# Kernel tuning notes

Measured on AMD Instinct MI355X. Metric: run time of the kernel, lower is better.

The kernel has to match this reference:

```python
import jax, jax.numpy as jnp
import numpy as np

N = 200_000        # atoms
E = 800_000        # directed edges (pairs e, e^1 are mutual reverses)
H = 512            # hidden_size
AF = 133           # atom_feat_size
BF = 14            # bond_feat_size
B = 4096           # num graphs


def setup_inputs() -> dict:
    key = jax.random.key(0)
    ks = jax.random.split(key, 8)
    atom_hiddens = jax.random.normal(ks[0], (N, H), dtype=jnp.float32)
    # undirected bonds, then interleave as (src,dst),(dst,src) so rev[e] = e ^ 1
    src = jax.random.randint(ks[1], (E // 2,), 0, N, dtype=jnp.int32)
    dst = jax.random.randint(ks[2], (E // 2,), 0, N, dtype=jnp.int32)
    heads = jnp.stack([src, dst], axis=1).reshape(-1)   # [E]
    tails = jnp.stack([dst, src], axis=1).reshape(-1)   # [E]
    edge_index = jnp.stack([heads, tails], axis=0)      # [2, E]
    rev_edge_index = jnp.arange(E, dtype=jnp.int32) ^ 1
    batch = jnp.sort(jax.random.randint(ks[3], (N,), 0, B, dtype=jnp.int32))
    batch = batch.at[-1].set(B - 1)  # batch[-1]+1 == B, matching the torch code
    s = 1.0 / np.sqrt(H)
    return {
        "atom_hiddens": atom_hiddens,
        "W_node": jax.random.normal(ks[4], (H, AF), dtype=jnp.float32) * s,
        "b_node": jnp.zeros((AF,), dtype=jnp.float32),
        "W_edge": jax.random.normal(ks[5], (H, BF), dtype=jnp.float32) * s,
        "b_edge": jnp.zeros((BF,), dtype=jnp.float32),
        "W_g1": jax.random.normal(ks[6], (H, H), dtype=jnp.float32) * s,
        "b_g1": jnp.zeros((H,), dtype=jnp.float32),
        "W_g2": jax.random.normal(ks[7], (H, 1), dtype=jnp.float32) * s,
        "b_g2": jnp.zeros((1,), dtype=jnp.float32),
        "edge_index": edge_index,
        "rev_edge_index": rev_edge_index,
        "batch": batch,
        "num_graphs": B,
    }


def reference(atom_hiddens, W_node, b_node, W_edge, b_edge, W_g1, b_g1,
              W_g2, b_g2, edge_index, rev_edge_index, batch, num_graphs):
    # graph pooling: index_add_ over the sorted batch vector
    graph_emb = jax.ops.segment_sum(atom_hiddens, batch, num_segments=num_graphs)
    # node head
    node_pred = atom_hiddens @ W_node + b_node
    # edge dedup: the torch loop keeps edge e iff its reverse was not yet
    # visited, i.e. iff e < rev_edge_index[e] (rev is an involution), giving
    # exactly E//2 kept edges.
    e_ids = jnp.arange(edge_index.shape[1])
    keep = jnp.nonzero(e_ids < rev_edge_index, size=edge_index.shape[1] // 2,
                       fill_value=0)[0]
    a1 = edge_index[0, keep]
    a2 = edge_index[1, keep]
    bond_emb = 0.5 * (atom_hiddens[a1] + atom_hiddens[a2])  # [E//2, H]
    edge_pred = bond_emb @ W_edge + b_edge
    # graph head: Linear -> ReLU -> Linear
    graph_pred = jax.nn.relu(graph_emb @ W_g1 + b_g1) @ W_g2 + b_g2
    return node_pred, edge_pred, graph_pred
```

## Files before the change

kernel.cpp:

```cpp
#include <hip/hip_runtime.h>

#define NATOMS 200000
#define NEDGE  800000
#define NBOND  400000
#define HDIM   512
#define AF     133
#define BFEAT  14
#define NGRAPH 4096

#define NODE_OUT_SZ (NATOMS * AF)
#define EDGE_OUT_SZ (NBOND * BFEAT)

#define WS_P     0
#define WS_BMAT  12800000
#define WS_BIAS  12963840
#define WS_GE    12964480
#define WS_WG1T  17158784

typedef _Float16 half8 __attribute__((ext_vector_type(8)));
typedef float floatx4 __attribute__((ext_vector_type(4)));

__global__ void pack_kernel(const float* __restrict__ Wn, const float* __restrict__ bn,
                            const float* __restrict__ We, const float* __restrict__ be,
                            const float* __restrict__ Wg1, const float* __restrict__ bg2,
                            _Float16* __restrict__ Bmat, float* __restrict__ bias,
                            _Float16* __restrict__ Wg1t, float* __restrict__ gpred) {
    int idx = blockIdx.x * 256 + threadIdx.x;
    if (idx < 160 * 512) {
        int n = idx >> 9, k = idx & 511;
        float v = 0.f;
        if (n < AF)              v = Wn[k * AF + n];
        else if (n < AF + BFEAT) v = We[k * BFEAT + (n - AF)];
        Bmat[idx] = (_Float16)v;
    } else if (idx < 160 * 512 + 512 * 512) {
        int i = idx - 160 * 512;
        int n = i >> 9, k = i & 511;
        Wg1t[i] = (_Float16)Wg1[k * HDIM + n];
    } else if (idx < 160 * 512 + 512 * 512 + 160) {
        int n = idx - (160 * 512 + 512 * 512);
        float v = 0.f;
        if (n < AF)              v = bn[n];
        else if (n < AF + BFEAT) v = be[n - AF];
        bias[n] = v;
    } else if (idx < 160 * 512 + 512 * 512 + 160 + NGRAPH) {
        gpred[idx - (160 * 512 + 512 * 512 + 160)] = bg2[0];
    }
}

__global__ __launch_bounds__(256) void pool_kernel(const float* __restrict__ A,
                                                   const int* __restrict__ batch,
                                                   _Float16* __restrict__ GE) {
    int g = blockIdx.x;
    int t = threadIdx.x;
    int lo = 0, hi = NATOMS;
    while (lo < hi) { int mid = (lo + hi) >> 1; if (batch[mid] < g) lo = mid + 1; else hi = mid; }
    int start = lo;
    hi = NATOMS;
    while (lo < hi) { int mid = (lo + hi) >> 1; if (batch[mid] < g + 1) lo = mid + 1; else hi = mid; }
    int end = lo;
    float s0 = 0.f, s1 = 0.f;
    for (int i = start; i < end; ++i) {
        s0 += A[(size_t)i * HDIM + t];
        s1 += A[(size_t)i * HDIM + t + 256];
    }
    GE[(size_t)g * HDIM + t]       = (_Float16)s0;
    GE[(size_t)g * HDIM + t + 256] = (_Float16)s1;
}

__global__ __launch_bounds__(256) void gemm_node(const float* __restrict__ A,
                                                 const _Float16* __restrict__ Bm,
                                                 const float* __restrict__ bias,
                                                 float* __restrict__ node_out,
                                                 float* __restrict__ P) {
    __shared__ _Float16 As[128][72];
    __shared__ _Float16 Bs[160][72];

    const int t    = threadIdx.x;
    const int bm   = blockIdx.x;
    const int w    = t >> 6, l = t & 63, quad = l >> 4, lr = l & 15;
    const int wm   = w & 1, wn = w >> 1;

    floatx4 acc[4][5];
    for (int mt = 0; mt < 4; ++mt)
        for (int nt = 0; nt < 5; ++nt)
            acc[mt][nt] = (floatx4){0.f, 0.f, 0.f, 0.f};

    const int arow0 = t >> 2;
    const int aseg  = (t & 3) * 16;

    for (int ko = 0; ko < 8; ++ko) {
        const int k0 = ko * 64;
        float4 av[2][4];
        for (int p = 0; p < 2; ++p) {
            int row = arow0 + p * 64;
            long grow = (long)bm * 128 + row;
            if (grow < NATOMS) {
                const float4* src = (const float4*)(A + grow * HDIM + k0 + aseg);
                av[p][0] = src[0]; av[p][1] = src[1]; av[p][2] = src[2]; av[p][3] = src[3];
            } else {
                av[p][0] = av[p][1] = av[p][2] = av[p][3] = make_float4(0.f, 0.f, 0.f, 0.f);
            }
        }
        uint4 bv[5];
        for (int it = 0; it < 5; ++it) {
            int idx = t + it * 256;
            int row = idx >> 3, c = (idx & 7) * 8;
            bv[it] = *(const uint4*)(Bm + row * HDIM + k0 + c);
        }
        __syncthreads();
        for (int p = 0; p < 2; ++p) {
            int row = arow0 + p * 64;
            half8 h0 = {(_Float16)av[p][0].x, (_Float16)av[p][0].y, (_Float16)av[p][0].z, (_Float16)av[p][0].w,
                        (_Float16)av[p][1].x, (_Float16)av[p][1].y, (_Float16)av[p][1].z, (_Float16)av[p][1].w};
            half8 h1 = {(_Float16)av[p][2].x, (_Float16)av[p][2].y, (_Float16)av[p][2].z, (_Float16)av[p][2].w,
                        (_Float16)av[p][3].x, (_Float16)av[p][3].y, (_Float16)av[p][3].z, (_Float16)av[p][3].w};
            *(half8*)&As[row][aseg]     = h0;
            *(half8*)&As[row][aseg + 8] = h1;
        }
        for (int it = 0; it < 5; ++it) {
            int idx = t + it * 256;
            int row = idx >> 3, c = (idx & 7) * 8;
            *(uint4*)&Bs[row][c] = bv[it];
        }
        __syncthreads();
        for (int kk = 0; kk < 64; kk += 32) {
            half8 af[4], bf[5];
            for (int mt = 0; mt < 4; ++mt)
                af[mt] = *(const half8*)&As[wm * 64 + mt * 16 + lr][kk + quad * 8];
            for (int nt = 0; nt < 5; ++nt)
                bf[nt] = *(const half8*)&Bs[wn * 80 + nt * 16 + lr][kk + quad * 8];
            for (int mt = 0; mt < 4; ++mt)
                for (int nt = 0; nt < 5; ++nt)
                    acc[mt][nt] = __builtin_amdgcn_mfma_f32_16x16x32_f16(af[mt], bf[nt], acc[mt][nt], 0, 0, 0);
        }
    }

    float biasv[5];
    for (int nt = 0; nt < 5; ++nt) biasv[nt] = bias[wn * 80 + nt * 16 + lr];
    for (int mt = 0; mt < 4; ++mt) {
        int rbase = bm * 128 + wm * 64 + mt * 16 + quad * 4;
        for (int r = 0; r < 4; ++r) {
            int grow = rbase + r;
            if (grow >= NATOMS) continue;
            for (int nt = 0; nt < 5; ++nt) {
                int gcol = wn * 80 + nt * 16 + lr;
                float v = acc[mt][nt][r] + biasv[nt];
                if (gcol < AF)                  node_out[(long)grow * AF + gcol] = v;
                else if (gcol < AF + BFEAT)     P[(long)grow * 16 + (gcol - AF)] = v;
            }
        }
    }
}

__global__ __launch_bounds__(256) void edge_kernel(const int* __restrict__ ei,
                                                   const float* __restrict__ P,
                                                   float* __restrict__ eout) {
    int t  = threadIdx.x;
    int j  = t & 15, bi = t >> 4;
    int b  = blockIdx.x * 16 + bi;
    if (b >= NBOND) return;
    if (j < BFEAT) {
        int e  = 2 * b;
        int a1 = ei[e];
        int a2 = ei[NEDGE + e];
        float v = 0.5f * (P[(size_t)a1 * 16 + j] + P[(size_t)a2 * 16 + j]);
        eout[(size_t)b * BFEAT + j] = v;
    }
}

__global__ __launch_bounds__(256) void gemm_graph(const _Float16* __restrict__ GE,
                                                  const _Float16* __restrict__ Bt,
                                                  const float* __restrict__ bg1,
                                                  const float* __restrict__ wg2,
                                                  float* __restrict__ gpred) {
    __shared__ _Float16 As[128][72];
    __shared__ _Float16 Bs[128][72];

    const int t   = threadIdx.x;
    const int bmb = blockIdx.x, bnb = blockIdx.y;
    const int w   = t >> 6, l = t & 63, quad = l >> 4, lr = l & 15;
    const int wm  = w & 1, wn = w >> 1;

    floatx4 acc[4][4];
    for (int mt = 0; mt < 4; ++mt)
        for (int nt = 0; nt < 4; ++nt)
            acc[mt][nt] = (floatx4){0.f, 0.f, 0.f, 0.f};

    for (int ko = 0; ko < 8; ++ko) {
        const int k0 = ko * 64;
        uint4 avv[4], bvv[4];
        for (int it = 0; it < 4; ++it) {
            int idx = t + it * 256;
            int row = idx >> 3, c = (idx & 7) * 8;
            avv[it] = *(const uint4*)(GE + (size_t)(bmb * 128 + row) * HDIM + k0 + c);
            bvv[it] = *(const uint4*)(Bt + (size_t)(bnb * 128 + row) * HDIM + k0 + c);
        }
        __syncthreads();
        for (int it = 0; it < 4; ++it) {
            int idx = t + it * 256;
            int row = idx >> 3, c = (idx & 7) * 8;
            *(uint4*)&As[row][c] = avv[it];
            *(uint4*)&Bs[row][c] = bvv[it];
        }
        __syncthreads();
        for (int kk = 0; kk < 64; kk += 32) {
            half8 af[4], bf[4];
            for (int mt = 0; mt < 4; ++mt)
                af[mt] = *(const half8*)&As[wm * 64 + mt * 16 + lr][kk + quad * 8];
            for (int nt = 0; nt < 4; ++nt)
                bf[nt] = *(const half8*)&Bs[wn * 64 + nt * 16 + lr][kk + quad * 8];
            for (int mt = 0; mt < 4; ++mt)
                for (int nt = 0; nt < 4; ++nt)
                    acc[mt][nt] = __builtin_amdgcn_mfma_f32_16x16x32_f16(af[mt], bf[nt], acc[mt][nt], 0, 0, 0);
        }
    }

    float bg1v[4], wg2v[4];
    for (int nt = 0; nt < 4; ++nt) {
        int col = bnb * 128 + wn * 64 + nt * 16 + lr;
        bg1v[nt] = bg1[col];
        wg2v[nt] = wg2[col];
    }
    for (int mt = 0; mt < 4; ++mt) {
        for (int r = 0; r < 4; ++r) {
            int row = bmb * 128 + wm * 64 + mt * 16 + quad * 4 + r;
            float partial = 0.f;
            for (int nt = 0; nt < 4; ++nt) {
                float v = acc[mt][nt][r] + bg1v[nt];
                v = v > 0.f ? v : 0.f;
                partial += v * wg2v[nt];
            }
            partial += __shfl_xor(partial, 1);
            partial += __shfl_xor(partial, 2);
            partial += __shfl_xor(partial, 4);
            partial += __shfl_xor(partial, 8);
            if (lr == 0) atomicAdd(&gpred[row], partial);
        }
    }
}

extern "C" void kernel_launch(void* const* d_in, const int* in_sizes, int n_in,
                              void* d_out, int out_size, void* d_ws, size_t ws_size,
                              hipStream_t stream) {
    const float* A    = (const float*)d_in[0];
    const float* Wn   = (const float*)d_in[1];
    const float* bn   = (const float*)d_in[2];
    const float* We   = (const float*)d_in[3];
    const float* be   = (const float*)d_in[4];
    const float* Wg1  = (const float*)d_in[5];
    const float* bg1  = (const float*)d_in[6];
    const float* Wg2  = (const float*)d_in[7];
    const float* bg2  = (const float*)d_in[8];
    const int*   ei   = (const int*)d_in[9];
    const int*   batch= (const int*)d_in[11];

    char* ws = (char*)d_ws;
    float*    P    = (float*)(ws + WS_P);
    _Float16* Bmat = (_Float16*)(ws + WS_BMAT);
    float*    bias = (float*)(ws + WS_BIAS);
    _Float16* GE   = (_Float16*)(ws + WS_GE);
    _Float16* Wg1t = (_Float16*)(ws + WS_WG1T);

    float* node_out = (float*)d_out;
    float* edge_out = node_out + NODE_OUT_SZ;
    float* gpred    = edge_out + EDGE_OUT_SZ;

    pack_kernel<<<dim3(1361), dim3(256), 0, stream>>>(Wn, bn, We, be, Wg1, bg2, Bmat, bias, Wg1t, gpred);
    pool_kernel<<<dim3(NGRAPH), dim3(256), 0, stream>>>(A, batch, GE);
    gemm_node<<<dim3((NATOMS + 127) / 128), dim3(256), 0, stream>>>(A, Bmat, bias, node_out, P);
    edge_kernel<<<dim3(NBOND / 16), dim3(256), 0, stream>>>(ei, P, edge_out);
    gemm_graph<<<dim3(32, 4), dim3(256), 0, stream>>>(GE, Wg1t, bg1, Wg2, gpred);
}
```

Before: 830.6 us.

## Fuse graph pooling into node GEMM via shared-memory segment sums and atomics

Removes the separate pool kernel, which re-read all of atom_hiddens (about 400 MB) from global memory. The node GEMM now also sums its fp16 A tiles already staged in LDS per graph segment and atomically adds the partials into an fp32 graph-embedding buffer. That buffer is zeroed by a new small kernel, and the graph GEMM reads it as fp32 and converts to fp16. The trade-offs are atomic traffic, extra LDS work inside the GEMM loop, and pooled sums built from fp16-rounded inputs rather than full fp32.

```diff
diff --git a/kernel.cpp b/kernel.cpp
--- a/kernel.cpp
+++ b/kernel.cpp
@@ -14,8 +14,8 @@
 #define WS_P     0
 #define WS_BMAT  12800000
 #define WS_BIAS  12963840
-#define WS_GE    12964480
-#define WS_WG1T  17158784
+#define WS_GEF   12964480
+#define WS_WG1T  21353088
 
 typedef _Float16 half8 __attribute__((ext_vector_type(8)));
 typedef float floatx4 __attribute__((ext_vector_type(4)));
@@ -47,39 +47,31 @@
     }
 }
 
-__global__ __launch_bounds__(256) void pool_kernel(const float* __restrict__ A,
-                                                   const int* __restrict__ batch,
-                                                   _Float16* __restrict__ GE) {
-    int g = blockIdx.x;
-    int t = threadIdx.x;
-    int lo = 0, hi = NATOMS;
-    while (lo < hi) { int mid = (lo + hi) >> 1; if (batch[mid] < g) lo = mid + 1; else hi = mid; }
-    int start = lo;
-    hi = NATOMS;
-    while (lo < hi) { int mid = (lo + hi) >> 1; if (batch[mid] < g + 1) lo = mid + 1; else hi = mid; }
-    int end = lo;
-    float s0 = 0.f, s1 = 0.f;
-    for (int i = start; i < end; ++i) {
-        s0 += A[(size_t)i * HDIM + t];
-        s1 += A[(size_t)i * HDIM + t + 256];
-    }
-    GE[(size_t)g * HDIM + t]       = (_Float16)s0;
-    GE[(size_t)g * HDIM + t + 256] = (_Float16)s1;
+__global__ void zero_ge(float4* __restrict__ GEf4) {
+    GEf4[blockIdx.x * 256 + threadIdx.x] = make_float4(0.f, 0.f, 0.f, 0.f);
 }
 
 __global__ __launch_bounds__(256) void gemm_node(const float* __restrict__ A,
                                                  const _Float16* __restrict__ Bm,
                                                  const float* __restrict__ bias,
+                                                 const int* __restrict__ batch,
                                                  float* __restrict__ node_out,
-                                                 float* __restrict__ P) {
+                                                 float* __restrict__ P,
+                                                 float* __restrict__ GEf) {
     __shared__ _Float16 As[128][72];
     __shared__ _Float16 Bs[160][72];
+    __shared__ int bg[128];
 
     const int t    = threadIdx.x;
     const int bm   = blockIdx.x;
     const int w    = t >> 6, l = t & 63, quad = l >> 4, lr = l & 15;
     const int wm   = w & 1, wn = w >> 1;
 
+    if (t < 128) {
+        int grow = bm * 128 + t;
+        bg[t] = (grow < NATOMS) ? batch[grow] : -1;
+    }
+
     floatx4 acc[4][5];
     for (int mt = 0; mt < 4; ++mt)
         for (int nt = 0; nt < 5; ++nt)
@@ -87,6 +79,8 @@
 
     const int arow0 = t >> 2;
     const int aseg  = (t & 3) * 16;
+    const int pc    = t & 63;
+    const int pq    = w;
 
     for (int ko = 0; ko < 8; ++ko) {
         const int k0 = ko * 64;
@@ -132,6 +126,19 @@
             for (int mt = 0; mt < 4; ++mt)
                 for (int nt = 0; nt < 5; ++nt)
                     acc[mt][nt] = __builtin_amdgcn_mfma_f32_16x16x32_f16(af[mt], bf[nt], acc[mt][nt], 0, 0, 0);
+        }
+        {
+            float psum = 0.f;
+            int pg = bg[pq * 32];
+            for (int r = pq * 32; r < pq * 32 + 32; ++r) {
+                int gid = bg[r];
+                if (gid != pg) {
+                    if (pg >= 0) atomicAdd(&GEf[(size_t)pg * HDIM + k0 + pc], psum);
+                    psum = 0.f; pg = gid;
+                }
+                psum += (float)As[r][pc];
+            }
+            if (pg >= 0) atomicAdd(&GEf[(size_t)pg * HDIM + k0 + pc], psum);
         }
     }
 
@@ -168,7 +175,7 @@
     }
 }
 
-__global__ __launch_bounds__(256) void gemm_graph(const _Float16* __restrict__ GE,
+__global__ __launch_bounds__(256) void gemm_graph(const float* __restrict__ GEf,
                                                   const _Float16* __restrict__ Bt,
                                                   const float* __restrict__ bg1,
                                                   const float* __restrict__ wg2,
@@ -186,20 +193,36 @@
         for (int nt = 0; nt < 4; ++nt)
             acc[mt][nt] = (floatx4){0.f, 0.f, 0.f, 0.f};
 
+    const int arow0 = t >> 2;
+    const int aseg  = (t & 3) * 16;
+
     for (int ko = 0; ko < 8; ++ko) {
         const int k0 = ko * 64;
-        uint4 avv[4], bvv[4];
+        float4 av[2][4];
+        for (int p = 0; p < 2; ++p) {
+            int row = bmb * 128 + arow0 + p * 64;
+            const float4* src = (const float4*)(GEf + (size_t)row * HDIM + k0 + aseg);
+            av[p][0] = src[0]; av[p][1] = src[1]; av[p][2] = src[2]; av[p][3] = src[3];
+        }
+        uint4 bvv[4];
         for (int it = 0; it < 4; ++it) {
             int idx = t + it * 256;
             int row = idx >> 3, c = (idx & 7) * 8;
-            avv[it] = *(const uint4*)(GE + (size_t)(bmb * 128 + row) * HDIM + k0 + c);
             bvv[it] = *(const uint4*)(Bt + (size_t)(bnb * 128 + row) * HDIM + k0 + c);
         }
         __syncthreads();
+        for (int p = 0; p < 2; ++p) {
+            int row = arow0 + p * 64;
+            half8 h0 = {(_Float16)av[p][0].x, (_Float16)av[p][0].y, (_Float16)av[p][0].z, (_Float16)av[p][0].w,
+                        (_Float16)av[p][1].x, (_Float16)av[p][1].y, (_Float16)av[p][1].z, (_Float16)av[p][1].w};
+            half8 h1 = {(_Float16)av[p][2].x, (_Float16)av[p][2].y, (_Float16)av[p][2].z, (_Float16)av[p][2].w,
+                        (_Float16)av[p][3].x, (_Float16)av[p][3].y, (_Float16)av[p][3].z, (_Float16)av[p][3].w};
+            *(half8*)&As[row][aseg]     = h0;
+            *(half8*)&As[row][aseg + 8] = h1;
+        }
         for (int it = 0; it < 4; ++it) {
             int idx = t + it * 256;
             int row = idx >> 3, c = (idx & 7) * 8;
-            *(uint4*)&As[row][c] = avv[it];
             *(uint4*)&Bs[row][c] = bvv[it];
         }
         __syncthreads();
@@ -258,7 +281,7 @@
     float*    P    = (float*)(ws + WS_P);
     _Float16* Bmat = (_Float16*)(ws + WS_BMAT);
     float*    bias = (float*)(ws + WS_BIAS);
-    _Float16* GE   = (_Float16*)(ws + WS_GE);
+    float*    GEf  = (float*)(ws + WS_GEF);
     _Float16* Wg1t = (_Float16*)(ws + WS_WG1T);
 
     float* node_out = (float*)d_out;
@@ -266,8 +289,8 @@
     float* gpred    = edge_out + EDGE_OUT_SZ;
 
     pack_kernel<<<dim3(1361), dim3(256), 0, stream>>>(Wn, bn, We, be, Wg1, bg2, Bmat, bias, Wg1t, gpred);
-    pool_kernel<<<dim3(NGRAPH), dim3(256), 0, stream>>>(A, batch, GE);
-    gemm_node<<<dim3((NATOMS + 127) / 128), dim3(256), 0, stream>>>(A, Bmat, bias, node_out, P);
+    zero_ge<<<dim3(NGRAPH * HDIM / 4 / 256), dim3(256), 0, stream>>>((float4*)GEf);
+    gemm_node<<<dim3((NATOMS + 127) / 128), dim3(256), 0, stream>>>(A, Bmat, bias, batch, node_out, P, GEf);
     edge_kernel<<<dim3(NBOND / 16), dim3(256), 0, stream>>>(ei, P, edge_out);
-    gemm_graph<<<dim3(32, 4), dim3(256), 0, stream>>>(GE, Wg1t, bg1, Wg2, gpred);
-}
+    gemm_graph<<<dim3(32, 4), dim3(256), 0, stream>>>(GEf, Wg1t, bg1, Wg2, gpred);
+}
```

Result: faster. 746.4 us (-10.1%).
